# Optimization experiments

Hardware: AMD Instinct MI355X
Metric: run time of the kernel (lower is better)

Reference implementation:

```python
import jax, jax.numpy as jnp
import numpy as np

TOKENS = 8192
MODEL_DIM = 4096
PROMPT_DIM = 64
NUM_EXPERTS = 8
TOP_K = 2
EPS = float(np.finfo(np.float32).eps)


def setup_inputs() -> dict:
    key = jax.random.key(0)
    k1, k2, k3 = jax.random.split(key, 3)
    x = jax.random.normal(k1, (TOKENS, MODEL_DIM), dtype=jnp.float32)
    prompt = jax.random.normal(k2, (TOKENS, PROMPT_DIM), dtype=jnp.float32)
    # gate linear: Linear(model_dim + prompt_dim, num_experts, bias=True)
    W = jax.random.normal(k3, (MODEL_DIM + PROMPT_DIM, NUM_EXPERTS), dtype=jnp.float32) * 0.02
    b = jnp.zeros((NUM_EXPERTS,), dtype=jnp.float32)
    return {"x": x, "prompt": prompt, "W": W, "b": b}


def reference(x, prompt, W, b):
    # eval path: no jitter, no noise (self.training is False)
    logits = jnp.concatenate([x, prompt], axis=-1) @ W + b          # [T, E]
    _, topk_idx = jax.lax.top_k(logits, TOP_K)                      # [T, K]
    masks = jax.nn.one_hot(topk_idx, NUM_EXPERTS, dtype=jnp.float32)  # [T, K, E]
    gates = jax.nn.softmax(logits, axis=-1)                         # [T, E]
    gates_s = jnp.einsum("te,tke->tk", gates, masks)               # masked gather-sum
    if TOP_K > 1:
        denom = jnp.maximum(gates_s.sum(axis=-1, keepdims=True), EPS)
        gates_s = gates_s / denom
    # masks[:, i] == masks_se[i], gates_s[:, i] == gates_s[i] in the torch code
    return masks, gates_s
```

## Files before the change

kernel.cpp:

```cpp
#include <hip/hip_runtime.h>
#include <math.h>

#define NE 8
#define KDIM 4096
#define PDIM 64
#define NQ 4
#define QK (KDIM / NQ)
#define TPB 16
#define LROW (QK + 16)
#define EPS_F32 1.1920929e-07f

typedef float f4 __attribute__((ext_vector_type(4)));

__global__ __launch_bounds__(256, 3)
void gate_partial(const float* __restrict__ x,
                  const float* __restrict__ prompt,
                  const float* __restrict__ W,
                  float* __restrict__ partials,
                  int tokens)
{
    const int tid   = threadIdx.x;
    const int lane  = tid & 63;
    const int wave  = tid >> 6;
    const int group = blockIdx.x >> 2;
    const int q     = blockIdx.x & 3;
    const int tbase = group * TPB + wave * 4;
    const int k0    = q * QK;

    __shared__ float lds_w[NE][LROW];

    f4 xv[4][4];
#pragma unroll
    for (int c = 0; c < 4; ++c)
#pragma unroll
        for (int t = 0; t < 4; ++t)
            xv[c][t] = __builtin_nontemporal_load(
                (const f4*)(x + (size_t)(tbase + t) * KDIM + k0 + c * 256 + lane * 4));

    const float* Wq = W + (size_t)k0 * NE;
#pragma unroll
    for (int it = 0; it < 8; ++it) {
        const int m  = it * 256 + tid;
        const f4 v   = *(const f4*)(Wq + 4 * m);
        const int kl = m >> 1;
        const int e0 = (m & 1) * 4;
        lds_w[e0 + 0][kl] = v.x;
        lds_w[e0 + 1][kl] = v.y;
        lds_w[e0 + 2][kl] = v.z;
        lds_w[e0 + 3][kl] = v.w;
    }
    __syncthreads();

    float acc[4][NE];
#pragma unroll
    for (int t = 0; t < 4; ++t)
#pragma unroll
        for (int e = 0; e < NE; ++e) acc[t][e] = 0.f;

#pragma unroll
    for (int c = 0; c < 4; ++c) {
        f4 wv[NE];
#pragma unroll
        for (int e = 0; e < NE; ++e)
            wv[e] = *(const f4*)(&lds_w[e][c * 256 + lane * 4]);
#pragma unroll
        for (int t = 0; t < 4; ++t)
#pragma unroll
            for (int e = 0; e < NE; ++e) {
                acc[t][e] = fmaf(xv[c][t].x, wv[e].x, acc[t][e]);
                acc[t][e] = fmaf(xv[c][t].y, wv[e].y, acc[t][e]);
                acc[t][e] = fmaf(xv[c][t].z, wv[e].z, acc[t][e]);
                acc[t][e] = fmaf(xv[c][t].w, wv[e].w, acc[t][e]);
            }
    }

    if (q == 3 && lane < 16) {
        const int k = lane * 4;
        f4 pv[4];
#pragma unroll
        for (int t = 0; t < 4; ++t)
            pv[t] = *(const f4*)(prompt + (size_t)(tbase + t) * PDIM + k);
        f4 wlo[4], whi[4];
#pragma unroll
        for (int j = 0; j < 4; ++j) {
            wlo[j] = *(const f4*)(W + (size_t)(KDIM + k + j) * NE);
            whi[j] = *(const f4*)(W + (size_t)(KDIM + k + j) * NE + 4);
        }
#pragma unroll
        for (int t = 0; t < 4; ++t) {
            const float* a = (const float*)&pv[t];
#pragma unroll
            for (int j = 0; j < 4; ++j) {
                acc[t][0] = fmaf(a[j], wlo[j].x, acc[t][0]);
                acc[t][1] = fmaf(a[j], wlo[j].y, acc[t][1]);
                acc[t][2] = fmaf(a[j], wlo[j].z, acc[t][2]);
                acc[t][3] = fmaf(a[j], wlo[j].w, acc[t][3]);
                acc[t][4] = fmaf(a[j], whi[j].x, acc[t][4]);
                acc[t][5] = fmaf(a[j], whi[j].y, acc[t][5]);
                acc[t][6] = fmaf(a[j], whi[j].z, acc[t][6]);
                acc[t][7] = fmaf(a[j], whi[j].w, acc[t][7]);
            }
        }
    }

#pragma unroll
    for (int t = 0; t < 4; ++t)
#pragma unroll
        for (int e = 0; e < NE; ++e) {
            float v = acc[t][e];
#pragma unroll
            for (int off = 32; off >= 1; off >>= 1)
                v += __shfl_xor(v, off, 64);
            acc[t][e] = v;
        }

    if (lane < 32) {
        const int t4 = lane >> 3;
        const int e  = lane & 7;
        partials[((size_t)q * tokens + tbase + t4) * NE + e] = acc[t4][e];
    }
}

__global__ __launch_bounds__(256)
void gate_epilogue(const float* __restrict__ partials,
                   const float* __restrict__ b,
                   float* __restrict__ out,
                   int tokens)
{
    const int tid   = threadIdx.x;
    const int lane  = tid & 63;
    const int wave  = tid >> 6;
    const int tbase = blockIdx.x * TPB + wave * 4;

    const int tt = lane >> 4;
    const int kk = (lane >> 3) & 1;
    const int ee = lane & 7;
    const int tg = tbase + tt;

    float lg[NE];
#pragma unroll
    for (int e = 0; e < NE; ++e) lg[e] = b[e];
#pragma unroll
    for (int qq = 0; qq < NQ; ++qq) {
        const f4 lo = *(const f4*)(partials + ((size_t)qq * tokens + tg) * NE);
        const f4 hi = *(const f4*)(partials + ((size_t)qq * tokens + tg) * NE + 4);
        lg[0] += lo.x; lg[1] += lo.y; lg[2] += lo.z; lg[3] += lo.w;
        lg[4] += hi.x; lg[5] += hi.y; lg[6] += hi.z; lg[7] += hi.w;
    }

    float v0 = lg[0]; int i0 = 0;
#pragma unroll
    for (int e = 1; e < NE; ++e)
        if (lg[e] > v0) { v0 = lg[e]; i0 = e; }
    float v1 = (i0 == 0) ? lg[1] : lg[0];
    int   i1 = (i0 == 0) ? 1 : 0;
#pragma unroll
    for (int e = 0; e < NE; ++e)
        if (e != i0 && lg[e] > v1) { v1 = lg[e]; i1 = e; }

    float s = 0.f;
#pragma unroll
    for (int e = 0; e < NE; ++e) s += __expf(lg[e] - v0);
    const float g0 = 1.0f / s;
    const float g1 = __expf(v1 - v0) / s;
    const float denom = fmaxf(g0 + g1, EPS_F32);

    const int sel = kk ? i1 : i0;
    out[(size_t)tg * 16 + kk * 8 + ee] = (ee == sel) ? 1.0f : 0.0f;

    if ((lane & 15) < 2) {
        const float g = (ee == 0) ? (g0 / denom) : (g1 / denom);
        out[(size_t)tokens * 16 + (size_t)tg * 2 + ee] = g;
    }
}

extern "C" void kernel_launch(void* const* d_in, const int* in_sizes, int n_in,
                              void* d_out, int out_size, void* d_ws, size_t ws_size,
                              hipStream_t stream) {
    const float* x      = (const float*)d_in[0];
    const float* prompt = (const float*)d_in[1];
    const float* W      = (const float*)d_in[2];
    const float* b      = (const float*)d_in[3];
    float* out          = (float*)d_out;
    float* partials     = (float*)d_ws;

    const int tokens = in_sizes[0] / KDIM;

    hipLaunchKernelGGL(gate_partial, dim3((tokens / TPB) * NQ), dim3(256), 0, stream,
                       x, prompt, W, partials, tokens);
    hipLaunchKernelGGL(gate_epilogue, dim3(tokens / TPB), dim3(256), 0, stream,
                       partials, b, out, tokens);
}
```

Before: 222.0 us.

## Halve K-split, enlarge blocks, and double-buffer x loads across K chunks

Splits K into two halves instead of four, with 512-thread blocks covering 32 tokens, and streams x through a two-deep register prefetch buffer across 8 chunks instead of loading all chunks up front. The prompt weight rows are staged in LDS, and fewer partial sums are written to and read back from global memory. The aim is to overlap x loads with FMA work and cut W staging and partial traffic. The larger LDS footprint per block limits residency, and each thread keeps fewer loads in flight, which may reduce memory parallelism.

After: 253.8 us. +14.3%, slower.

```diff
diff --git a/kernel.cpp b/kernel.cpp
--- a/kernel.cpp
+++ b/kernel.cpp
@@ -4,15 +4,14 @@
 #define NE 8
 #define KDIM 4096
 #define PDIM 64
-#define NQ 4
+#define NQ 2
 #define QK (KDIM / NQ)
-#define TPB 16
 #define LROW (QK + 16)
 #define EPS_F32 1.1920929e-07f
 
 typedef float f4 __attribute__((ext_vector_type(4)));
 
-__global__ __launch_bounds__(256, 3)
+__global__ __launch_bounds__(512, 4)
 void gate_partial(const float* __restrict__ x,
                   const float* __restrict__ prompt,
                   const float* __restrict__ W,
@@ -22,25 +21,18 @@
     const int tid   = threadIdx.x;
     const int lane  = tid & 63;
     const int wave  = tid >> 6;
-    const int group = blockIdx.x >> 2;
-    const int q     = blockIdx.x & 3;
-    const int tbase = group * TPB + wave * 4;
+    const int group = blockIdx.x >> 1;
+    const int q     = blockIdx.x & 1;
+    const int tbase = group * 32 + wave * 4;
     const int k0    = q * QK;
 
     __shared__ float lds_w[NE][LROW];
-
-    f4 xv[4][4];
-#pragma unroll
-    for (int c = 0; c < 4; ++c)
-#pragma unroll
-        for (int t = 0; t < 4; ++t)
-            xv[c][t] = __builtin_nontemporal_load(
-                (const f4*)(x + (size_t)(tbase + t) * KDIM + k0 + c * 256 + lane * 4));
+    __shared__ float lds_wp[NE][68];
 
     const float* Wq = W + (size_t)k0 * NE;
 #pragma unroll
     for (int it = 0; it < 8; ++it) {
-        const int m  = it * 256 + tid;
+        const int m  = it * 512 + tid;
         const f4 v   = *(const f4*)(Wq + 4 * m);
         const int kl = m >> 1;
         const int e0 = (m & 1) * 4;
@@ -49,6 +41,25 @@
         lds_w[e0 + 2][kl] = v.z;
         lds_w[e0 + 3][kl] = v.w;
     }
+    if (q == 1 && tid < 128) {
+        const f4 v   = *(const f4*)(W + (size_t)KDIM * NE + 4 * tid);
+        const int kl = tid >> 1;
+        const int e0 = (tid & 1) * 4;
+        lds_wp[e0 + 0][kl] = v.x;
+        lds_wp[e0 + 1][kl] = v.y;
+        lds_wp[e0 + 2][kl] = v.z;
+        lds_wp[e0 + 3][kl] = v.w;
+    }
+
+    const float* xw = x + (size_t)tbase * KDIM + k0 + lane * 4;
+    f4 xv[2][4];
+#pragma unroll
+    for (int s = 0; s < 2; ++s)
+#pragma unroll
+        for (int t = 0; t < 4; ++t)
+            xv[s][t] = __builtin_nontemporal_load(
+                (const f4*)(xw + (size_t)t * KDIM + s * 256));
+
     __syncthreads();
 
     float acc[4][NE];
@@ -58,48 +69,56 @@
         for (int e = 0; e < NE; ++e) acc[t][e] = 0.f;
 
 #pragma unroll
-    for (int c = 0; c < 4; ++c) {
-        f4 wv[NE];
-#pragma unroll
-        for (int e = 0; e < NE; ++e)
-            wv[e] = *(const f4*)(&lds_w[e][c * 256 + lane * 4]);
-#pragma unroll
-        for (int t = 0; t < 4; ++t)
-#pragma unroll
-            for (int e = 0; e < NE; ++e) {
-                acc[t][e] = fmaf(xv[c][t].x, wv[e].x, acc[t][e]);
-                acc[t][e] = fmaf(xv[c][t].y, wv[e].y, acc[t][e]);
-                acc[t][e] = fmaf(xv[c][t].z, wv[e].z, acc[t][e]);
-                acc[t][e] = fmaf(xv[c][t].w, wv[e].w, acc[t][e]);
-            }
-    }
-
-    if (q == 3 && lane < 16) {
+    for (int s = 0; s < 8; ++s) {
+        const int cur = s & 1;
+        const int kl  = s * 256 + lane * 4;
+#pragma unroll
+        for (int eh = 0; eh < 2; ++eh) {
+            f4 wv[4];
+#pragma unroll
+            for (int j = 0; j < 4; ++j)
+                wv[j] = *(const f4*)(&lds_w[eh * 4 + j][kl]);
+#pragma unroll
+            for (int t = 0; t < 4; ++t)
+#pragma unroll
+                for (int j = 0; j < 4; ++j) {
+                    const int e = eh * 4 + j;
+                    acc[t][e] = fmaf(xv[cur][t].x, wv[j].x, acc[t][e]);
+                    acc[t][e] = fmaf(xv[cur][t].y, wv[j].y, acc[t][e]);
+                    acc[t][e] = fmaf(xv[cur][t].z, wv[j].z, acc[t][e]);
+                    acc[t][e] = fmaf(xv[cur][t].w, wv[j].w, acc[t][e]);
+                }
+        }
+        if (s + 2 < 8) {
+#pragma unroll
+            for (int t = 0; t < 4; ++t)
+                xv[cur][t] = __builtin_nontemporal_load(
+                    (const f4*)(xw + (size_t)t * KDIM + (s + 2) * 256));
+        }
+    }
+
+    if (q == 1 && lane < 16) {
         const int k = lane * 4;
         f4 pv[4];
 #pragma unroll
         for (int t = 0; t < 4; ++t)
             pv[t] = *(const f4*)(prompt + (size_t)(tbase + t) * PDIM + k);
-        f4 wlo[4], whi[4];
-#pragma unroll
-        for (int j = 0; j < 4; ++j) {
-            wlo[j] = *(const f4*)(W + (size_t)(KDIM + k + j) * NE);
-            whi[j] = *(const f4*)(W + (size_t)(KDIM + k + j) * NE + 4);
-        }
-#pragma unroll
-        for (int t = 0; t < 4; ++t) {
-            const float* a = (const float*)&pv[t];
-#pragma unroll
-            for (int j = 0; j < 4; ++j) {
-                acc[t][0] = fmaf(a[j], wlo[j].x, acc[t][0]);
-                acc[t][1] = fmaf(a[j], wlo[j].y, acc[t][1]);
-                acc[t][2] = fmaf(a[j], wlo[j].z, acc[t][2]);
-                acc[t][3] = fmaf(a[j], wlo[j].w, acc[t][3]);
-                acc[t][4] = fmaf(a[j], whi[j].x, acc[t][4]);
-                acc[t][5] = fmaf(a[j], whi[j].y, acc[t][5]);
-                acc[t][6] = fmaf(a[j], whi[j].z, acc[t][6]);
-                acc[t][7] = fmaf(a[j], whi[j].w, acc[t][7]);
-            }
+#pragma unroll
+        for (int eh = 0; eh < 2; ++eh) {
+            f4 wv[4];
+#pragma unroll
+            for (int j = 0; j < 4; ++j)
+                wv[j] = *(const f4*)(&lds_wp[eh * 4 + j][k]);
+#pragma unroll
+            for (int t = 0; t < 4; ++t)
+#pragma unroll
+                for (int j = 0; j < 4; ++j) {
+                    const int e = eh * 4 + j;
+                    acc[t][e] = fmaf(pv[t].x, wv[j].x, acc[t][e]);
+                    acc[t][e] = fmaf(pv[t].y, wv[j].y, acc[t][e]);
+                    acc[t][e] = fmaf(pv[t].z, wv[j].z, acc[t][e]);
+                    acc[t][e] = fmaf(pv[t].w, wv[j].w, acc[t][e]);
+                }
         }
     }
 
@@ -130,7 +149,7 @@
     const int tid   = threadIdx.x;
     const int lane  = tid & 63;
     const int wave  = tid >> 6;
-    const int tbase = blockIdx.x * TPB + wave * 4;
+    const int tbase = blockIdx.x * 16 + wave * 4;
 
     const int tt = lane >> 4;
     const int kk = (lane >> 3) & 1;
@@ -186,8 +205,8 @@
 
     const int tokens = in_sizes[0] / KDIM;
 
-    hipLaunchKernelGGL(gate_partial, dim3((tokens / TPB) * NQ), dim3(256), 0, stream,
+    hipLaunchKernelGGL(gate_partial, dim3((tokens / 32) * NQ), dim3(512), 0, stream,
                        x, prompt, W, partials, tokens);
-    hipLaunchKernelGGL(gate_epilogue, dim3(tokens / TPB), dim3(256), 0, stream,
+    hipLaunchKernelGGL(gate_epilogue, dim3(tokens / 16), dim3(256), 0, stream,
                        partials, b, out, tokens);
 }
```
